# Optimization experiments

Measured on AMD Instinct MI355X. Metric: run time of the kernel, lower is better.

Reference implementation:

```python
import jax, jax.numpy as jnp
import numpy as np

DIM, E, K = 256, 8, 2
B, D, H, W = 1, 32, 32, 32
EPS = 1e-5


def setup_inputs() -> dict:
    key = jax.random.key(0)
    ks = jax.random.split(key, 16)
    nrm = lambda k, s, sc=0.02: jax.random.normal(k, s, jnp.float32) * sc
    def resblock_params(k):
        k1, k2, k3, k4 = jax.random.split(k, 4)
        return dict(
            c1w=nrm(k1, (DIM, DIM, 3, 3, 3)), c1b=jnp.zeros((DIM,), jnp.float32),
            g1=jax.random.uniform(k2, (DIM,), jnp.float32, 0.5, 1.5), be1=jnp.zeros((DIM,), jnp.float32),
            c2w=nrm(k3, (DIM, DIM, 3, 3, 3)), c2b=jnp.zeros((DIM,), jnp.float32),
            g2=jax.random.uniform(k4, (DIM,), jnp.float32, 0.5, 1.5), be2=jnp.zeros((DIM,), jnp.float32),
        )
    p1 = resblock_params(ks[5])
    p2 = resblock_params(ks[6])
    return {
        "x": jax.random.normal(ks[0], (B, DIM, D, H, W), jnp.float32),
        "wg": nrm(ks[1], (DIM, E)),
        "w1": nrm(ks[2], (E, DIM, DIM)), "b1": jnp.zeros((E, DIM), jnp.float32),
        "w2": nrm(ks[3], (E, DIM, DIM)), "b2": jnp.zeros((E, DIM), jnp.float32),
        "r1_c1w": p1["c1w"], "r1_c1b": p1["c1b"], "r1_g1": p1["g1"], "r1_be1": p1["be1"],
        "r1_c2w": p1["c2w"], "r1_c2b": p1["c2b"], "r1_g2": p1["g2"], "r1_be2": p1["be2"],
        "r2_c1w": p2["c1w"], "r2_c1b": p2["c1b"], "r2_g1": p2["g1"], "r2_be1": p2["be1"],
        "r2_c2w": p2["c2w"], "r2_c2b": p2["c2b"], "r2_g2": p2["g2"], "r2_be2": p2["be2"],
        "c8w": nrm(ks[4], (DIM, DIM, 1, 1, 1)), "c8b": jnp.zeros((DIM,), jnp.float32),
    }


def conv3d(x, w, b, pad):
    y = jax.lax.conv_general_dilated(
        x, w, window_strides=(1, 1, 1), padding=[(pad, pad)] * 3,
        dimension_numbers=("NCDHW", "OIDHW", "NCDHW"))
    return y + b[None, :, None, None, None]


def batchnorm(x, g, b):
    m = x.mean(axis=(0, 2, 3, 4), keepdims=True)
    v = x.var(axis=(0, 2, 3, 4), keepdims=True)
    return g[None, :, None, None, None] * (x - m) * jax.lax.rsqrt(v + EPS) + b[None, :, None, None, None]


def unet_res_block(x, c1w, c1b, g1, be1, c2w, c2b, g2, be2):
    out = jax.nn.leaky_relu(batchnorm(conv3d(x, c1w, c1b, 1), g1, be1), 0.01)
    out = batchnorm(conv3d(out, c2w, c2b, 1), g2, be2)
    return jax.nn.leaky_relu(out + x, 0.01)  # identity shortcut (in==out ch, stride 1)


def mom_block(x, wg, w1, b1, w2, b2):
    Bb, C, Dd, Hh, Ww = x.shape
    tokens = x.transpose(0, 2, 3, 4, 1).reshape(-1, C)  # [T, C]
    T = tokens.shape[0]
    probs = jax.nn.softmax(tokens @ wg, axis=-1)          # [T, E]
    vals, idx = jax.lax.top_k(probs, K)                   # [T, K]
    wts = vals / vals.sum(-1, keepdims=True)
    gates = jnp.zeros((T, E), probs.dtype).at[jnp.arange(T)[:, None], idx].set(wts)
    # dense expert MLPs (math-equivalent to gather/dispatch/combine)
    h = jax.nn.gelu(jnp.einsum("tc,ech->eth", tokens, w1) + b1[:, None, :])
    eo = jnp.einsum("eth,ehc->etc", h, w2) + b2[:, None, :]
    moe = jnp.einsum("te,etc->tc", gates, eo)             # [T, C]
    # switch-style load-balancing auxiliary loss
    density = (gates > 0).astype(probs.dtype).mean(0)     # fraction of tokens per expert
    density_proxy = probs.mean(0)
    aux = (density * density_proxy).sum() * E
    out = x + moe.reshape(Bb, Dd, Hh, Ww, C).transpose(0, 4, 1, 2, 3)
    return out, aux


def reference(x, wg, w1, b1, w2, b2,
              r1_c1w, r1_c1b, r1_g1, r1_be1, r1_c2w, r1_c2b, r1_g2, r1_be2,
              r2_c1w, r2_c1b, r2_g1, r2_be1, r2_c2w, r2_c2b, r2_g2, r2_be2,
              c8w, c8b):
    xm, aux = mom_block(x, wg, w1, b1, w2, b2)
    res = unet_res_block(xm, r1_c1w, r1_c1b, r1_g1, r1_be1, r1_c2w, r1_c2b, r1_g2, r1_be2)
    res = unet_res_block(res, r2_c1w, r2_c1b, r2_g1, r2_be1, r2_c2w, r2_c2b, r2_g2, r2_be2)
    out = xm + conv3d(res, c8w, c8b, 0)  # Dropout3d is identity at eval
    return out, aux
```

## Files before the change

### kernel.cpp

```cpp
#include <hip/hip_runtime.h>
#include <stdint.h>

typedef __attribute__((ext_vector_type(8))) short short8;
typedef __attribute__((ext_vector_type(4))) float f32x4;
typedef unsigned short u16;
typedef unsigned int u32;
typedef unsigned long long u64;

#define WS_TOK   0ull
#define WS_XT    16777216ull
#define WS_XMCT  50331648ull
#define WS_GATES 83886080ull
#define WS_H     84934656ull
#define WS_P1    135266304ull
#define WS_P2    155389952ull
#define WS_Y     175513600ull
#define WS_R2    209068032ull
#define WS_WRB   225845248ull
#define WS_W1P   240001024ull
#define WS_W2P   241049600ull
#define WS_C8P   242098176ull
#define WS_PART  242229248ull
#define WS_SF    243277824ull
#define WS_AUXP  243279872ull

#define WS_PERM  (WS_H + 0x00000ull)
#define WS_TBL   (WS_H + 0x60000ull)
#define WS_META  (WS_H + 0x70000ull)
#define WS_BCNT  (WS_H + 0x80000ull)
#define WS_BOFF  (WS_H + 0x90000ull)
#define WS_SEL   (WS_H + 0x100000ull)

__device__ __forceinline__ u16 f2bf(float f) {
  u32 x = __float_as_uint(f);
  u32 r = x + 0x7fffu + ((x >> 16) & 1u);
  return (u16)(r >> 16);
}

__global__ void trans_in_k(const float* __restrict__ x, float* __restrict__ xt,
                           u16* __restrict__ tok) {
  __shared__ float ld[64][65];
  int tt = blockIdx.x, cc = blockIdx.y, tid = threadIdx.x;
#pragma unroll
  for (int k = 0; k < 16; ++k) {
    int idx = tid + k * 256;
    int cl = idx >> 6, j = idx & 63;
    ld[cl][j] = x[(size_t)(cc * 64 + cl) * 32768 + tt * 64 + j];
  }
  __syncthreads();
#pragma unroll
  for (int k = 0; k < 16; ++k) {
    int idx = tid + k * 256;
    int tl = idx >> 6, cl = idx & 63;
    float v = ld[cl][tl];
    size_t o = (size_t)(tt * 64 + tl) * 256 + cc * 64 + cl;
    xt[o] = v;
    tok[o] = f2bf(v);
  }
}

__global__ void pack_rb_k(const float* __restrict__ w0, const float* __restrict__ w1,
                          const float* __restrict__ w2, const float* __restrict__ w3,
                          u16* __restrict__ out) {
  __shared__ float ld[6912];
  int conv = blockIdx.x >> 8, blk = blockIdx.x & 255, tid = threadIdx.x;
  const float* src = conv == 0 ? w0 : conv == 1 ? w1 : conv == 2 ? w2 : w3;
  size_t base = (size_t)blk * 256 * 27;
#pragma unroll
  for (int k = 0; k < 27; ++k) ld[tid + k * 256] = src[base + tid + k * 256];
  __syncthreads();
  u16* dst = out + (size_t)conv * 27 * 65536;
  int n = blk * 256 + tid;
#pragma unroll
  for (int tap = 0; tap < 27; ++tap)
    dst[(size_t)tap * 65536 + n] = f2bf(ld[tid * 27 + tap]);
}

__global__ void pack_tr_k(const float* __restrict__ w1, const float* __restrict__ w2,
                          u16* __restrict__ w1p, u16* __restrict__ w2p) {
  __shared__ float ld[64][65];
  int m = blockIdx.y, tile = blockIdx.x, tid = threadIdx.x;
  const float* src = (m < 8) ? (w1 + (size_t)m * 65536) : (w2 + (size_t)(m - 8) * 65536);
  u16* dst = (m < 8) ? (w1p + (size_t)m * 65536) : (w2p + (size_t)(m - 8) * 65536);
  int r0 = (tile >> 2) * 64, c0 = (tile & 3) * 64;
#pragma unroll
  for (int k = 0; k < 16; ++k) {
    int idx = tid + k * 256;
    int rr = idx >> 6, cc = idx & 63;
    ld[rr][cc] = src[(size_t)(r0 + rr) * 256 + c0 + cc];
  }
  __syncthreads();
#pragma unroll
  for (int k = 0; k < 16; ++k) {
    int idx = tid + k * 256;
    int cc = idx >> 6, rr = idx & 63;
    dst[(size_t)(c0 + cc) * 256 + r0 + rr] = f2bf(ld[rr][cc]);
  }
}

__global__ void cvt_k(const float* __restrict__ in, u16* __restrict__ out, int n) {
  int i = blockIdx.x * 256 + threadIdx.x;
  if (i < n) out[i] = f2bf(in[i]);
}

__global__ void halo_k(u16* __restrict__ P1, u16* __restrict__ P2) {
  int gid = blockIdx.x * 256 + threadIdx.x;
  int r = gid >> 5, o = (gid & 31) << 3;
  if (r >= 39304) return;
  int d = r / 1156, rem = r - d * 1156, h = rem / 34, w = rem - h * 34;
  if (d >= 1 && d <= 32 && h >= 1 && h <= 32 && w >= 1 && w <= 32) return;
  uint4 z = {0u, 0u, 0u, 0u};
  *(uint4*)(P1 + (size_t)r * 256 + o) = z;
  *(uint4*)(P2 + (size_t)r * 256 + o) = z;
}

__global__ void gate_k(const float* __restrict__ xt, const float* __restrict__ wg,
                       float* __restrict__ gw, u32* __restrict__ sel,
                       u32* __restrict__ blk_cnt, float* __restrict__ auxp) {
  __shared__ float wgs[2048];
  __shared__ float ax[4][16];
  __shared__ u32 bc[4][8];
  int tid = threadIdx.x;
#pragma unroll
  for (int k = 0; k < 8; ++k) wgs[tid + k * 256] = wg[tid + k * 256];
  __syncthreads();
  int t = blockIdx.x * 256 + tid;
  int lane = tid & 63, wv = tid >> 6;
  float l[8] = {0, 0, 0, 0, 0, 0, 0, 0};
  const float* xr = xt + (size_t)t * 256;
  for (int c = 0; c < 256; c += 4) {
    float4 xv = *(const float4*)(xr + c);
#pragma unroll
    for (int e = 0; e < 8; ++e)
      l[e] += xv.x * wgs[c * 8 + e] + xv.y * wgs[(c + 1) * 8 + e] +
              xv.z * wgs[(c + 2) * 8 + e] + xv.w * wgs[(c + 3) * 8 + e];
  }
  float mx = l[0];
#pragma unroll
  for (int e = 1; e < 8; ++e) mx = fmaxf(mx, l[e]);
  float p[8], sum = 0.f;
#pragma unroll
  for (int e = 0; e < 8; ++e) { p[e] = __expf(l[e] - mx); sum += p[e]; }
  float inv = 1.0f / sum;
#pragma unroll
  for (int e = 0; e < 8; ++e) p[e] *= inv;
  int i0 = 0; float v0 = p[0];
#pragma unroll
  for (int e = 1; e < 8; ++e) if (p[e] > v0) { v0 = p[e]; i0 = e; }
  int i1 = -1; float v1 = -1.0f;
#pragma unroll
  for (int e = 0; e < 8; ++e) if (e != i0 && p[e] > v1) { v1 = p[e]; i1 = e; }
  float wsum = v0 + v1;
  gw[t * 2] = v0 / wsum;
  gw[t * 2 + 1] = v1 / wsum;
  sel[t] = (u32)i0 | ((u32)i1 << 4);
  u64 mm[8];
#pragma unroll
  for (int e = 0; e < 8; ++e) mm[e] = __ballot(i0 == e || i1 == e);
  if (lane == 0) {
#pragma unroll
    for (int e = 0; e < 8; ++e) bc[wv][e] = (u32)__popcll(mm[e]);
  }
#pragma unroll
  for (int e = 0; e < 8; ++e) {
    float ps = p[e];
    float cn = (e == i0 || e == i1) ? 1.0f : 0.0f;
    for (int o = 32; o; o >>= 1) { ps += __shfl_down(ps, o); cn += __shfl_down(cn, o); }
    if (lane == 0) { ax[wv][e] = ps; ax[wv][8 + e] = cn; }
  }
  __syncthreads();
  if (tid < 16)
    auxp[blockIdx.x * 16 + tid] = ax[0][tid] + ax[1][tid] + ax[2][tid] + ax[3][tid];
  if (tid < 8)
    blk_cnt[blockIdx.x * 8 + tid] = bc[0][tid] + bc[1][tid] + bc[2][tid] + bc[3][tid];
}

__global__ void aux_k(const float* __restrict__ auxp, float* __restrict__ out) {
  __shared__ float s[16];
  int i = threadIdx.x;
  if (i < 16) {
    float a = 0;
    for (int b = 0; b < 128; ++b) a += auxp[b * 16 + i];
    s[i] = a;
  }
  __syncthreads();
  if (i == 0) {
    float r = 0;
    for (int e = 0; e < 8; ++e)
      r += (s[8 + e] * (1.0f / 32768.0f)) * (s[e] * (1.0f / 32768.0f));
    out[0] = r * 8.0f;
  }
}

__global__ void scan_k(const u32* __restrict__ blk_cnt, u32* __restrict__ blkoff,
                       u32* __restrict__ tbl, u32* __restrict__ meta,
                       u32* __restrict__ perm) {
  __shared__ u32 tot[8], base[8], nck[8], cbase[8];
  int tid = threadIdx.x;
  if (tid < 8) {
    u32 run = 0;
    for (int b = 0; b < 128; ++b) {
      blkoff[b * 8 + tid] = run;
      run += blk_cnt[b * 8 + tid];
    }
    tot[tid] = run;
  }
  __syncthreads();
  if (tid == 0) {
    u32 acc = 0, c = 0;
    for (int e = 0; e < 8; ++e) {
      base[e] = acc;
      u32 nc = (tot[e] + 127) >> 7;
      nck[e] = nc;
      cbase[e] = c;
      acc += nc << 7;
      c += nc;
    }
    meta[0] = c;
  }
  __syncthreads();
  for (int i = tid; i < 1024; i += 256) blkoff[i] += base[i & 7];
  if (tid < 8) {
    for (u32 k = 0; k < nck[tid]; ++k)
      tbl[cbase[tid] + k] = ((base[tid] + (k << 7)) << 4) | (u32)tid;
    for (u32 sl = base[tid] + tot[tid]; sl < base[tid] + (nck[tid] << 7); ++sl)
      perm[sl] = 0;
  }
}

__global__ void scatter_k(const u32* __restrict__ sel, const u32* __restrict__ blkoff,
                          u32* __restrict__ perm, u32* __restrict__ tpos) {
  __shared__ u32 wcnt[4][8];
  int tid = threadIdx.x, b = blockIdx.x;
  int lane = tid & 63, wv = tid >> 6;
  int t = b * 256 + tid;
  u32 s = sel[t];
  int i0 = s & 15, i1 = (s >> 4) & 15;
  u64 mm[8];
#pragma unroll
  for (int e = 0; e < 8; ++e) mm[e] = __ballot(i0 == e || i1 == e);
  if (lane == 0) {
#pragma unroll
    for (int e = 0; e < 8; ++e) wcnt[wv][e] = (u32)__popcll(mm[e]);
  }
  __syncthreads();
  u64 lt = (1ull << lane) - 1ull;
#pragma unroll
  for (int e = 0; e < 8; ++e) {
    bool is0 = (i0 == e), is1 = (i1 == e);
    if (is0 || is1) {
      u32 woff = 0;
#pragma unroll
      for (int w = 0; w < 4; ++w)
        if (w < wv) woff += wcnt[w][e];
      u32 pos = blkoff[b * 8 + e] + woff + (u32)__popcll(mm[e] & lt);
      perm[pos] = (u32)t;
      tpos[t * 2 + (is0 ? 0 : 1)] = pos;
    }
  }
}

__global__ __launch_bounds__(512, 2) void moe_gemm_k(
    const u16* __restrict__ tok, const u32* __restrict__ perm,
    const u32* __restrict__ tbl, const u32* __restrict__ meta,
    const u16* __restrict__ w1p, const u16* __restrict__ w2p,
    const float* __restrict__ b1, const float* __restrict__ b2,
    u16* __restrict__ eo) {
  __shared__ __attribute__((aligned(16))) unsigned char smem[163840];
  const int bid = blockIdx.x;
  if ((u32)bid >= meta[0]) return;
  const u32 ent = tbl[bid];
  const int e = (int)(ent & 15u);
  const int slot0 = (int)(ent >> 4);
  const int tid = threadIdx.x;
  const int lane = tid & 63;
  const int wv = tid >> 6;
  const int wr = (wv >> 2) * 64;
  const int wc = (wv & 3) * 64;
  const int fq = lane >> 4, fr = lane & 15;
  const u16* w1e = w1p + e * 65536;
  const u16* w2e = w2p + e * 65536;

#pragma unroll
  for (int it = 0; it < 8; ++it) {
    int s = tid + it * 512;
    int r = s >> 5, seg = s & 31;
    int cole = ((seg >> 3) << 6) + (((seg & 7) ^ (r & 7)) << 3);
    u32 rowtok = perm[slot0 + r];
    __builtin_amdgcn_global_load_lds(
        (const __attribute__((address_space(1))) u32*)(tok + (size_t)rowtok * 256 + cole),
        (__attribute__((address_space(3))) u32*)(smem + s * 16), 16, 0, 0);
  }

  f32x4 acc1[4][4];
#pragma unroll
  for (int mc = 0; mc < 4; ++mc)
#pragma unroll
    for (int nt = 0; nt < 4; ++nt) acc1[mc][nt] = (f32x4){0.f, 0.f, 0.f, 0.f};

#pragma unroll 1
  for (int kc = 0; kc < 4; ++kc) {
#pragma unroll
    for (int it = 0; it < 4; ++it) {
      int s = tid + it * 512;
      int r = s >> 3;
      int sub = (s & 7) ^ (r & 7);
      __builtin_amdgcn_global_load_lds(
          (const __attribute__((address_space(1))) u32*)(w1e + (size_t)r * 256 + kc * 64 + sub * 8),
          (__attribute__((address_space(3))) u32*)(smem + 65536 + s * 16), 16, 0, 0);
    }
    __syncthreads();
#pragma unroll
    for (int khf = 0; khf < 2; ++khf) {
      short8 af1[4], bt[4];
#pragma unroll
      for (int mc = 0; mc < 4; ++mc) {
        int row = wc + mc * 16 + fr;
        int p = (khf * 4 + fq) ^ (row & 7);
        af1[mc] = *(const short8*)(smem + 65536 + row * 128 + p * 16);
      }
#pragma unroll
      for (int nt = 0; nt < 4; ++nt) {
        int row = wr + nt * 16 + fr;
        int p = (khf * 4 + fq) ^ (row & 7);
        bt[nt] = *(const short8*)(smem + row * 512 + kc * 128 + p * 16);
      }
#pragma unroll
      for (int mc = 0; mc < 4; ++mc)
#pragma unroll
        for (int nt = 0; nt < 4; ++nt)
          acc1[mc][nt] = __builtin_amdgcn_mfma_f32_16x16x32_bf16(af1[mc], bt[nt], acc1[mc][nt], 0, 0, 0);
    }
    __syncthreads();
  }

#pragma unroll
  for (int mc = 0; mc < 4; ++mc) {
    int k0 = wc + mc * 16 + fq * 4;
    float4 bv = *(const float4*)(b1 + e * 256 + k0);
#pragma unroll
    for (int nt = 0; nt < 4; ++nt) {
      int t = wr + nt * 16 + fr;
      u64 pk = 0;
#pragma unroll
      for (int j = 0; j < 4; ++j) {
        float v = acc1[mc][nt][j] + ((const float*)&bv)[j];
        float u = 1.5957691216057308f * (v + 0.044715f * v * v * v);
        float g = v / (1.0f + __expf(-u));
        pk |= (u64)f2bf(g) << (16 * j);
      }
      *(u64*)(smem + 98304 + t * 512 + ((k0 * 2) ^ ((t & 7) << 4))) = pk;
    }
  }

  f32x4 acc2[4][4];
#pragma unroll
  for (int m = 0; m < 4; ++m)
#pragma unroll
    for (int n = 0; n < 4; ++n) acc2[m][n] = (f32x4){0.f, 0.f, 0.f, 0.f};

#pragma unroll 1
  for (int kc = 0; kc < 4; ++kc) {
#pragma unroll
    for (int it = 0; it < 4; ++it) {
      int s = tid + it * 512;
      int r = s >> 3;
      int sub = (s & 7) ^ (r & 7);
      __builtin_amdgcn_global_load_lds(
          (const __attribute__((address_space(1))) u32*)(w2e + (size_t)r * 256 + kc * 64 + sub * 8),
          (__attribute__((address_space(3))) u32*)(smem + 65536 + s * 16), 16, 0, 0);
    }
    __syncthreads();
#pragma unroll
    for (int khf = 0; khf < 2; ++khf) {
      short8 af[4], bb[4];
#pragma unroll
      for (int m = 0; m < 4; ++m) {
        int row = wr + m * 16 + fr;
        int col = (kc * 128 + (khf * 4 + fq) * 16) ^ ((row & 7) << 4);
        af[m] = *(const short8*)(smem + 98304 + row * 512 + col);
      }
#pragma unroll
      for (int n = 0; n < 4; ++n) {
        int row = wc + n * 16 + fr;
        int p = (khf * 4 + fq) ^ (row & 7);
        bb[n] = *(const short8*)(smem + 65536 + row * 128 + p * 16);
      }
#pragma unroll
      for (int m = 0; m < 4; ++m)
#pragma unroll
        for (int n = 0; n < 4; ++n)
          acc2[m][n] = __builtin_amdgcn_mfma_f32_16x16x32_bf16(af[m], bb[n], acc2[m][n], 0, 0, 0);
    }
    __syncthreads();
  }

  float bs2[4];
#pragma unroll
  for (int n = 0; n < 4; ++n) bs2[n] = b2[e * 256 + wc + n * 16 + fr];
#pragma unroll
  for (int m = 0; m < 4; ++m)
#pragma unroll
    for (int j = 0; j < 4; ++j) {
      int rowslot = slot0 + wr + m * 16 + fq * 4 + j;
      u16* er = eo + (size_t)rowslot * 256 + wc;
#pragma unroll
      for (int n = 0; n < 4; ++n) er[n * 16 + fr] = f2bf(acc2[m][n][j] + bs2[n]);
    }
}

__global__ void combine_k(float* __restrict__ xt, const u16* __restrict__ eo,
                          const float* __restrict__ gw, const u32* __restrict__ tpos,
                          float* __restrict__ xmct, u16* __restrict__ pad) {
  __shared__ float ld[64][65];
  __shared__ u32 pp[64][2];
  __shared__ float gg[64][2];
  int tt = blockIdx.x, cc = blockIdx.y, tid = threadIdx.x;
  if (tid < 128) {
    int tl = tid >> 1, s = tid & 1;
    int t = tt * 64 + tl;
    pp[tl][s] = tpos[t * 2 + s];
    gg[tl][s] = gw[t * 2 + s];
  }
  __syncthreads();
#pragma unroll
  for (int k = 0; k < 16; ++k) {
    int idx = tid + k * 256;
    int tl = idx >> 6, cl = idx & 63;
    int c = cc * 64 + cl;
    size_t o = (size_t)(tt * 64 + tl) * 256 + c;
    float e0 = __uint_as_float((u32)eo[(size_t)pp[tl][0] * 256 + c] << 16);
    float e1 = __uint_as_float((u32)eo[(size_t)pp[tl][1] * 256 + c] << 16);
    float v = xt[o] + gg[tl][0] * e0 + gg[tl][1] * e1;
    xt[o] = v;
    ld[tl][cl] = v;
    int t = tt * 64 + tl;
    int d = t >> 10, h = (t >> 5) & 31, w = t & 31;
    int prow = (d + 1) * 1156 + (h + 1) * 34 + (w + 1);
    pad[(size_t)prow * 256 + c] = f2bf(v);
  }
  __syncthreads();
#pragma unroll
  for (int k = 0; k < 16; ++k) {
    int idx = tid + k * 256;
    int cl = idx >> 6, tl = idx & 63;
    xmct[(size_t)(cc * 64 + cl) * 32768 + tt * 64 + tl] = ld[tl][cl];
  }
}

template <int MODE>
__global__ __launch_bounds__(256, 2) void gemm_k(
    const u16* __restrict__ A, const u16* __restrict__ Bw,
    const float* __restrict__ bias, float* __restrict__ outF,
    const float* __restrict__ xmct, float* __restrict__ part) {
  __shared__ __attribute__((aligned(16))) unsigned char smem[65536];
  const int tid = threadIdx.x;
  const int bx = blockIdx.x;
  const int ttile = (MODE == 0) ? ((bx & 7) * 32 + (bx >> 3)) : bx;
  const int ctile = blockIdx.y;
  const int lane = tid & 63;
  const int wv = tid >> 6;
  const int wr = (wv >> 1) << 6;
  const int wc = (wv & 1) << 6;
  const int fq = lane >> 4;
  const int fr = lane & 15;

  int aoff[4], boff[4];
#pragma unroll
  for (int it = 0; it < 4; ++it) {
    int s = tid + it * 256;
    int r = s >> 3;
    int lsg = (s & 7) ^ (r & 7);
    if (MODE == 0) {
      int dd = ttile >> 3;
      int h0 = (ttile & 7) << 2;
      int base = dd * 1156 + (h0 + (r >> 5)) * 34 + (r & 31);
      aoff[it] = base * 256 + lsg * 8;
    } else {
      aoff[it] = (ttile * 128 + r) * 256 + lsg * 8;
    }
    boff[it] = (ctile * 128 + r) * 256 + lsg * 8;
  }

  f32x4 acc[4][4];
#pragma unroll
  for (int m = 0; m < 4; ++m)
#pragma unroll
    for (int n = 0; n < 4; ++n) acc[m][n] = (f32x4){0.f, 0.f, 0.f, 0.f};

  const int nStep = (MODE == 0) ? 108 : 4;

  auto stage = [&](int s, int buf) {
    int tap = (MODE == 0) ? (s >> 2) : 0;
    int kc = s & 3;
    int atap = 0, btap = 0;
    if (MODE == 0) {
      atap = ((tap / 9) * 1156 + ((tap / 3) % 3) * 34 + (tap % 3)) * 256;
      btap = tap * 65536;
    }
    const u16* Ak = A + atap + kc * 64;
    const u16* Bk = Bw + btap + kc * 64;
    unsigned char* sb = smem + buf * 32768;
#pragma unroll
    for (int it = 0; it < 4; ++it) {
      __builtin_amdgcn_global_load_lds(
          (const __attribute__((address_space(1))) u32*)(Ak + aoff[it]),
          (__attribute__((address_space(3))) u32*)(sb + (tid + it * 256) * 16),
          16, 0, 0);
      __builtin_amdgcn_global_load_lds(
          (const __attribute__((address_space(1))) u32*)(Bk + boff[it]),
          (__attribute__((address_space(3))) u32*)(sb + 16384 + (tid + it * 256) * 16),
          16, 0, 0);
    }
  };

  auto compute = [&](int buf) {
    unsigned char* sb = smem + buf * 32768;
#pragma unroll
    for (int khf = 0; khf < 2; ++khf) {
      short8 af[4], bb[4];
#pragma unroll
      for (int m = 0; m < 4; ++m) {
        int row = wr + m * 16 + fr;
        int p = (khf * 4 + fq) ^ (row & 7);
        af[m] = *(const short8*)(sb + row * 128 + p * 16);
      }
#pragma unroll
      for (int n = 0; n < 4; ++n) {
        int row = wc + n * 16 + fr;
        int p = (khf * 4 + fq) ^ (row & 7);
        bb[n] = *(const short8*)(sb + 16384 + row * 128 + p * 16);
      }
#pragma unroll
      for (int m = 0; m < 4; ++m)
#pragma unroll
        for (int n = 0; n < 4; ++n)
          acc[m][n] = __builtin_amdgcn_mfma_f32_16x16x32_bf16(af[m], bb[n], acc[m][n], 0, 0, 0);
    }
  };

  stage(0, 0);
  asm volatile("s_waitcnt vmcnt(0)" ::: "memory");
  __builtin_amdgcn_s_barrier();
  int cur = 0;
#pragma unroll 1
  for (int s = 0; s < nStep; ++s) {
    if (s + 1 < nStep) stage(s + 1, cur ^ 1);
    compute(cur);
    asm volatile("s_waitcnt vmcnt(0)" ::: "memory");
    __builtin_amdgcn_s_barrier();
    cur ^= 1;
  }

  float bs[4];
#pragma unroll
  for (int n = 0; n < 4; ++n) bs[n] = bias[ctile * 128 + wc + n * 16 + fr];

  if (MODE == 3) {
#pragma unroll
    for (int m = 0; m < 4; ++m) {
      int trow = ttile * 128 + wr + m * 16 + fq * 4;
#pragma unroll
      for (int n = 0; n < 4; ++n) {
        int oc = ctile * 128 + wc + n * 16 + fr;
        size_t o = (size_t)oc * 32768 + trow;
        float4 xv = *(const float4*)(xmct + o);
        float4 w;
        w.x = acc[m][n][0] + bs[n] + xv.x;
        w.y = acc[m][n][1] + bs[n] + xv.y;
        w.z = acc[m][n][2] + bs[n] + xv.z;
        w.w = acc[m][n][3] + bs[n] + xv.w;
        *(float4*)(outF + o) = w;
      }
    }
  } else {
    float sn[4] = {0, 0, 0, 0}, qn[4] = {0, 0, 0, 0};
#pragma unroll
    for (int m = 0; m < 4; ++m) {
#pragma unroll
      for (int j = 0; j < 4; ++j) {
        int t = ttile * 128 + wr + m * 16 + fq * 4 + j;
        float* yr = outF + (size_t)t * 256 + ctile * 128 + wc;
#pragma unroll
        for (int n = 0; n < 4; ++n) {
          float v = acc[m][n][j] + bs[n];
          yr[n * 16 + fr] = v;
          sn[n] += v;
          qn[n] += v * v;
        }
      }
    }
#pragma unroll
    for (int n = 0; n < 4; ++n) {
      float s = sn[n], q = qn[n];
      s += __shfl_xor(s, 16); s += __shfl_xor(s, 32);
      q += __shfl_xor(q, 16); q += __shfl_xor(q, 32);
      if (lane < 16) {
        int pi = (ttile * 2 + (wv >> 1)) * 256 + ctile * 128 + wc + n * 16 + fr;
        part[pi] = s;
        part[131072 + pi] = q;
      }
    }
  }
}

__global__ void stats2_k(const float* __restrict__ part, const float* __restrict__ g,
                         const float* __restrict__ be, float* __restrict__ sf) {
  __shared__ float sred[4][256], qred[4][256];
  int tid = threadIdx.x;
  int c = tid & 255, qd = tid >> 8;
  float s = 0, q = 0;
  for (int b = qd * 128; b < qd * 128 + 128; ++b) {
    s += part[b * 256 + c];
    q += part[131072 + b * 256 + c];
  }
  sred[qd][c] = s;
  qred[qd][c] = q;
  __syncthreads();
  if (qd == 0) {
    s = sred[0][c] + sred[1][c] + sred[2][c] + sred[3][c];
    q = qred[0][c] + qred[1][c] + qred[2][c] + qred[3][c];
    float mean = s * (1.0f / 32768.0f);
    float var = q * (1.0f / 32768.0f) - mean * mean;
    float a = g[c] * rsqrtf(var + 1e-5f);
    sf[c] = a;
    sf[256 + c] = be[c] - mean * a;
  }
}

template <int V>
__global__ void bn_k(const float* __restrict__ y, const float* __restrict__ sf,
                     const float* __restrict__ skip, u16* __restrict__ pad,
                     float* __restrict__ f32o, u16* __restrict__ bfo) {
  int gid = blockIdx.x * 256 + threadIdx.x;
  int t = gid >> 5, c0 = (gid & 31) << 3;
  size_t base = (size_t)t * 256 + c0;
  float v[8];
  const float4* yp = (const float4*)(y + base);
  float4 y0 = yp[0], y1 = yp[1];
  const float4* ap = (const float4*)(sf + c0);
  float4 a0 = ap[0], a1 = ap[1];
  const float4* shp = (const float4*)(sf + 256 + c0);
  float4 s0 = shp[0], s1 = shp[1];
  v[0] = a0.x * y0.x + s0.x; v[1] = a0.y * y0.y + s0.y;
  v[2] = a0.z * y0.z + s0.z; v[3] = a0.w * y0.w + s0.w;
  v[4] = a1.x * y1.x + s1.x; v[5] = a1.y * y1.y + s1.y;
  v[6] = a1.z * y1.z + s1.z; v[7] = a1.w * y1.w + s1.w;
  if (V >= 1) {
    const float4* kp = (const float4*)(skip + base);
    float4 k0 = kp[0], k1 = kp[1];
    v[0] += k0.x; v[1] += k0.y; v[2] += k0.z; v[3] += k0.w;
    v[4] += k1.x; v[5] += k1.y; v[6] += k1.z; v[7] += k1.w;
  }
#pragma unroll
  for (int i = 0; i < 8; ++i) v[i] = v[i] > 0.0f ? v[i] : 0.01f * v[i];
  if (V <= 1) {
    int d = t >> 10, h = (t >> 5) & 31, w = t & 31;
    int prow = (d + 1) * 1156 + (h + 1) * 34 + (w + 1);
    uint4 pk;
    pk.x = (u32)f2bf(v[0]) | ((u32)f2bf(v[1]) << 16);
    pk.y = (u32)f2bf(v[2]) | ((u32)f2bf(v[3]) << 16);
    pk.z = (u32)f2bf(v[4]) | ((u32)f2bf(v[5]) << 16);
    pk.w = (u32)f2bf(v[6]) | ((u32)f2bf(v[7]) << 16);
    *(uint4*)(pad + (size_t)prow * 256 + c0) = pk;
  }
  if (V == 1) {
    float4 o0 = {v[0], v[1], v[2], v[3]}, o1 = {v[4], v[5], v[6], v[7]};
    float4* fp = (float4*)(f32o + base);
    fp[0] = o0; fp[1] = o1;
  }
  if (V == 2) {
    uint4 pk;
    pk.x = (u32)f2bf(v[0]) | ((u32)f2bf(v[1]) << 16);
    pk.y = (u32)f2bf(v[2]) | ((u32)f2bf(v[3]) << 16);
    pk.z = (u32)f2bf(v[4]) | ((u32)f2bf(v[5]) << 16);
    pk.w = (u32)f2bf(v[6]) | ((u32)f2bf(v[7]) << 16);
    *(uint4*)(bfo + base) = pk;
  }
}

extern "C" void kernel_launch(void* const* d_in, const int* in_sizes, int n_in,
                              void* d_out, int out_size, void* d_ws, size_t ws_size,
                              hipStream_t stream) {
  (void)in_sizes; (void)n_in; (void)out_size; (void)ws_size;
  const float* x  = (const float*)d_in[0];
  const float* wg = (const float*)d_in[1];
  const float* w1 = (const float*)d_in[2];
  const float* b1 = (const float*)d_in[3];
  const float* w2 = (const float*)d_in[4];
  const float* b2 = (const float*)d_in[5];

  char* ws = (char*)d_ws;
  u16* tok    = (u16*)(ws + WS_TOK);
  float* xt   = (float*)(ws + WS_XT);
  float* xmct = (float*)(ws + WS_XMCT);
  float* gw   = (float*)(ws + WS_GATES);
  u32* tpos   = (u32*)(ws + WS_GATES + 0x80000ull);
  u32* perm   = (u32*)(ws + WS_PERM);
  u32* tbl    = (u32*)(ws + WS_TBL);
  u32* meta   = (u32*)(ws + WS_META);
  u32* bcnt   = (u32*)(ws + WS_BCNT);
  u32* boff   = (u32*)(ws + WS_BOFF);
  u32* selb   = (u32*)(ws + WS_SEL);
  u16* P1     = (u16*)(ws + WS_P1);
  u16* P2     = (u16*)(ws + WS_P2);
  float* ybuf = (float*)(ws + WS_Y);
  u16* eo     = (u16*)(ws + WS_Y);
  u16* r2b    = (u16*)(ws + WS_R2);
  u16* wrb    = (u16*)(ws + WS_WRB);
  u16* w1p    = (u16*)(ws + WS_W1P);
  u16* w2p    = (u16*)(ws + WS_W2P);
  u16* c8p    = (u16*)(ws + WS_C8P);
  float* part = (float*)(ws + WS_PART);
  float* sf   = (float*)(ws + WS_SF);
  float* auxp = (float*)(ws + WS_AUXP);
  float* outp = (float*)d_out;

  halo_k<<<4913, 256, 0, stream>>>(P1, P2);
  trans_in_k<<<dim3(512, 4), 256, 0, stream>>>(x, xt, tok);
  pack_rb_k<<<1024, 256, 0, stream>>>((const float*)d_in[6], (const float*)d_in[10],
                                      (const float*)d_in[14], (const float*)d_in[18], wrb);
  pack_tr_k<<<dim3(16, 16), 256, 0, stream>>>(w1, w2, w1p, w2p);
  cvt_k<<<256, 256, 0, stream>>>((const float*)d_in[22], c8p, 65536);

  gate_k<<<128, 256, 0, stream>>>(xt, wg, gw, selb, bcnt, auxp);
  scan_k<<<1, 256, 0, stream>>>(bcnt, boff, tbl, meta, perm);
  scatter_k<<<128, 256, 0, stream>>>(selb, boff, perm, tpos);
  moe_gemm_k<<<520, 512, 0, stream>>>(tok, perm, tbl, meta, w1p, w2p, b1, b2, eo);
  combine_k<<<dim3(512, 4), 256, 0, stream>>>(xt, eo, gw, tpos, xmct, P1);

  gemm_k<0><<<dim3(256, 2), 256, 0, stream>>>(P1, wrb + 0 * 1769472, (const float*)d_in[7],
                                              ybuf, nullptr, part);
  stats2_k<<<1, 1024, 0, stream>>>(part, (const float*)d_in[8], (const float*)d_in[9], sf);
  bn_k<0><<<4096, 256, 0, stream>>>(ybuf, sf, nullptr, P2, nullptr, nullptr);
  gemm_k<0><<<dim3(256, 2), 256, 0, stream>>>(P2, wrb + 1 * 1769472, (const float*)d_in[11],
                                              ybuf, nullptr, part);
  stats2_k<<<1, 1024, 0, stream>>>(part, (const float*)d_in[12], (const float*)d_in[13], sf);
  bn_k<1><<<4096, 256, 0, stream>>>(ybuf, sf, xt, P1, xt, nullptr);

  gemm_k<0><<<dim3(256, 2), 256, 0, stream>>>(P1, wrb + 2 * 1769472, (const float*)d_in[15],
                                              ybuf, nullptr, part);
  stats2_k<<<1, 1024, 0, stream>>>(part, (const float*)d_in[16], (const float*)d_in[17], sf);
  bn_k<0><<<4096, 256, 0, stream>>>(ybuf, sf, nullptr, P2, nullptr, nullptr);
  gemm_k<0><<<dim3(256, 2), 256, 0, stream>>>(P2, wrb + 3 * 1769472, (const float*)d_in[19],
                                              ybuf, nullptr, part);
  stats2_k<<<1, 1024, 0, stream>>>(part, (const float*)d_in[20], (const float*)d_in[21], sf);
  bn_k<2><<<4096, 256, 0, stream>>>(ybuf, sf, xt, nullptr, nullptr, r2b);

  gemm_k<3><<<dim3(256, 2), 256, 0, stream>>>(r2b, c8p, (const float*)d_in[23], outp,
                                              xmct, nullptr);
  aux_k<<<1, 64, 0, stream>>>(auxp, outp + 8388608);
}
```

Measured before the change: 713.8 us.

## Widen conv GEMM to full 256 output channels with triple-buffered pipeline and bf16 output

Replaces the 3x3x3 conv GEMM with a dedicated 512-thread kernel that computes all 256 output channels per token tile. This halves redundant loads of the padded activation tile, and each stage's global-to-LDS loads are split across the two k-halves behind a three-deep buffer ring, with MFMA priority raised. The conv output is now stored as bf16 instead of fp32, which halves intermediate traffic read back by the batchnorm kernel. The trade-off is lower BN input precision, one block per CU with heavy LDS use, and fewer blocks (256) to fill the device.

```diff
diff --git a/kernel.cpp b/kernel.cpp
--- a/kernel.cpp
+++ b/kernel.cpp
@@ -36,6 +36,7 @@
   u32 r = x + 0x7fffu + ((x >> 16) & 1u);
   return (u16)(r >> 16);
 }
+__device__ __forceinline__ float bf2f(u32 u) { return __uint_as_float(u << 16); }
 
 __global__ void trans_in_k(const float* __restrict__ x, float* __restrict__ xt,
                            u16* __restrict__ tok) {
@@ -429,8 +430,8 @@
     int tl = idx >> 6, cl = idx & 63;
     int c = cc * 64 + cl;
     size_t o = (size_t)(tt * 64 + tl) * 256 + c;
-    float e0 = __uint_as_float((u32)eo[(size_t)pp[tl][0] * 256 + c] << 16);
-    float e1 = __uint_as_float((u32)eo[(size_t)pp[tl][1] * 256 + c] << 16);
+    float e0 = bf2f(eo[(size_t)pp[tl][0] * 256 + c]);
+    float e1 = bf2f(eo[(size_t)pp[tl][1] * 256 + c]);
     float v = xt[o] + gg[tl][0] * e0 + gg[tl][1] * e1;
     xt[o] = v;
     ld[tl][cl] = v;
@@ -448,15 +449,159 @@
   }
 }
 
-template <int MODE>
-__global__ __launch_bounds__(256, 2) void gemm_k(
+__global__ __launch_bounds__(512, 1) void conv_k(
+    const u16* __restrict__ P, const u16* __restrict__ W,
+    const float* __restrict__ bias, u16* __restrict__ y,
+    float* __restrict__ part) {
+  __shared__ __attribute__((aligned(16))) unsigned char smem[147456];
+  const int tid = threadIdx.x;
+  const int bx = blockIdx.x;
+  const int ttile = (bx & 7) * 32 + (bx >> 3);
+  const int lane = tid & 63;
+  const int wv = tid >> 6;
+  const int wr = (wv >> 2) << 6;
+  const int wc = (wv & 3) << 6;
+  const int fq = lane >> 4, fr = lane & 15;
+  const int dd = ttile >> 3, h0 = (ttile & 7) << 2;
+
+  int goffA[2];
+#pragma unroll
+  for (int it = 0; it < 2; ++it) {
+    int s = tid + it * 512;
+    int r = s >> 3, c = s & 7;
+    int base = dd * 1156 + (h0 + (r >> 5)) * 34 + (r & 31);
+    goffA[it] = base * 256 + ((c ^ (r & 7)) << 3);
+  }
+  int goffB[4];
+#pragma unroll
+  for (int it = 0; it < 4; ++it) {
+    int s = tid + it * 512;
+    int r = s >> 3, c = s & 7;
+    goffB[it] = r * 256 + ((c ^ (r & 7)) << 3);
+  }
+
+  f32x4 acc[4][4];
+#pragma unroll
+  for (int m = 0; m < 4; ++m)
+#pragma unroll
+    for (int n = 0; n < 4; ++n) acc[m][n] = (f32x4){0.f, 0.f, 0.f, 0.f};
+
+#define CONV_STAGE(s2, half)                                                        \
+  {                                                                                 \
+    int tap_ = (s2) >> 2, kc_ = (s2) & 3;                                           \
+    int aofs_ = ((tap_ / 9) * 1156 + ((tap_ / 3) % 3) * 34 + (tap_ % 3)) * 256 +    \
+                kc_ * 64;                                                           \
+    int bofs_ = tap_ * 65536 + kc_ * 64;                                            \
+    unsigned char* sb_ = smem + ((s2) % 3) * 49152;                                 \
+    if ((half) == 0) {                                                              \
+      __builtin_amdgcn_global_load_lds(                                             \
+          (const __attribute__((address_space(1))) u32*)(P + aofs_ + goffA[0]),     \
+          (__attribute__((address_space(3))) u32*)(sb_ + tid * 16), 16, 0, 0);      \
+      __builtin_amdgcn_global_load_lds(                                             \
+          (const __attribute__((address_space(1))) u32*)(P + aofs_ + goffA[1]),     \
+          (__attribute__((address_space(3))) u32*)(sb_ + (tid + 512) * 16), 16, 0, 0); \
+      __builtin_amdgcn_global_load_lds(                                             \
+          (const __attribute__((address_space(1))) u32*)(W + bofs_ + goffB[0]),     \
+          (__attribute__((address_space(3))) u32*)(sb_ + 16384 + tid * 16), 16, 0, 0); \
+    } else {                                                                        \
+      __builtin_amdgcn_global_load_lds(                                             \
+          (const __attribute__((address_space(1))) u32*)(W + bofs_ + goffB[1]),     \
+          (__attribute__((address_space(3))) u32*)(sb_ + 16384 + (tid + 512) * 16), \
+          16, 0, 0);                                                                \
+      __builtin_amdgcn_global_load_lds(                                             \
+          (const __attribute__((address_space(1))) u32*)(W + bofs_ + goffB[2]),     \
+          (__attribute__((address_space(3))) u32*)(sb_ + 16384 + (tid + 1024) * 16),\
+          16, 0, 0);                                                                \
+      __builtin_amdgcn_global_load_lds(                                             \
+          (const __attribute__((address_space(1))) u32*)(W + bofs_ + goffB[3]),     \
+          (__attribute__((address_space(3))) u32*)(sb_ + 16384 + (tid + 1536) * 16),\
+          16, 0, 0);                                                                \
+    }                                                                               \
+  }
+
+  CONV_STAGE(0, 0); CONV_STAGE(0, 1);
+  CONV_STAGE(1, 0); CONV_STAGE(1, 1);
+  asm volatile("s_waitcnt vmcnt(6)" ::: "memory");
+  __builtin_amdgcn_s_barrier();
+
+#pragma unroll 1
+  for (int s = 0; s < 108; ++s) {
+    const unsigned char* sb = smem + (s % 3) * 49152;
+    const bool doStage = (s < 106);
+#pragma unroll
+    for (int khf = 0; khf < 2; ++khf) {
+      short8 af[4], bb[4];
+#pragma unroll
+      for (int m = 0; m < 4; ++m) {
+        int row = wr + m * 16 + fr;
+        int p = (khf * 4 + fq) ^ (row & 7);
+        af[m] = *(const short8*)(sb + row * 128 + p * 16);
+      }
+#pragma unroll
+      for (int n = 0; n < 4; ++n) {
+        int row = wc + n * 16 + fr;
+        int p = (khf * 4 + fq) ^ (row & 7);
+        bb[n] = *(const short8*)(sb + 16384 + row * 128 + p * 16);
+      }
+      if (doStage) CONV_STAGE(s + 2, khf);
+      __builtin_amdgcn_s_barrier();
+      __builtin_amdgcn_s_setprio(1);
+#pragma unroll
+      for (int m = 0; m < 4; ++m)
+#pragma unroll
+        for (int n = 0; n < 4; ++n)
+          acc[m][n] = __builtin_amdgcn_mfma_f32_16x16x32_bf16(af[m], bb[n], acc[m][n], 0, 0, 0);
+      __builtin_amdgcn_s_setprio(0);
+      if (khf == 0) __builtin_amdgcn_s_barrier();
+    }
+    if (doStage)
+      asm volatile("s_waitcnt vmcnt(6)" ::: "memory");
+    else
+      asm volatile("s_waitcnt vmcnt(0)" ::: "memory");
+    __builtin_amdgcn_s_barrier();
+  }
+#undef CONV_STAGE
+
+  float bs[4];
+#pragma unroll
+  for (int n = 0; n < 4; ++n) bs[n] = bias[wc + n * 16 + fr];
+
+  float sn[4] = {0, 0, 0, 0}, qn[4] = {0, 0, 0, 0};
+#pragma unroll
+  for (int m = 0; m < 4; ++m) {
+#pragma unroll
+    for (int j = 0; j < 4; ++j) {
+      int t = ttile * 128 + wr + m * 16 + fq * 4 + j;
+      u16* yr = y + (size_t)t * 256 + wc;
+#pragma unroll
+      for (int n = 0; n < 4; ++n) {
+        float v = acc[m][n][j] + bs[n];
+        yr[n * 16 + fr] = f2bf(v);
+        sn[n] += v;
+        qn[n] += v * v;
+      }
+    }
+  }
+#pragma unroll
+  for (int n = 0; n < 4; ++n) {
+    float s = sn[n], q = qn[n];
+    s += __shfl_xor(s, 16); s += __shfl_xor(s, 32);
+    q += __shfl_xor(q, 16); q += __shfl_xor(q, 32);
+    if (lane < 16) {
+      int pi = (ttile * 2 + (wv >> 2)) * 256 + wc + n * 16 + fr;
+      part[pi] = s;
+      part[131072 + pi] = q;
+    }
+  }
+}
+
+__global__ __launch_bounds__(256, 2) void final_k(
     const u16* __restrict__ A, const u16* __restrict__ Bw,
     const float* __restrict__ bias, float* __restrict__ outF,
-    const float* __restrict__ xmct, float* __restrict__ part) {
+    const float* __restrict__ xmct) {
   __shared__ __attribute__((aligned(16))) unsigned char smem[65536];
   const int tid = threadIdx.x;
-  const int bx = blockIdx.x;
-  const int ttile = (MODE == 0) ? ((bx & 7) * 32 + (bx >> 3)) : bx;
+  const int ttile = blockIdx.x;
   const int ctile = blockIdx.y;
   const int lane = tid & 63;
   const int wv = tid >> 6;
@@ -471,14 +616,7 @@
     int s = tid + it * 256;
     int r = s >> 3;
     int lsg = (s & 7) ^ (r & 7);
-    if (MODE == 0) {
-      int dd = ttile >> 3;
-      int h0 = (ttile & 7) << 2;
-      int base = dd * 1156 + (h0 + (r >> 5)) * 34 + (r & 31);
-      aoff[it] = base * 256 + lsg * 8;
-    } else {
-      aoff[it] = (ttile * 128 + r) * 256 + lsg * 8;
-    }
+    aoff[it] = (ttile * 128 + r) * 256 + lsg * 8;
     boff[it] = (ctile * 128 + r) * 256 + lsg * 8;
   }
 
@@ -488,18 +626,9 @@
 #pragma unroll
     for (int n = 0; n < 4; ++n) acc[m][n] = (f32x4){0.f, 0.f, 0.f, 0.f};
 
-  const int nStep = (MODE == 0) ? 108 : 4;
-
-  auto stage = [&](int s, int buf) {
-    int tap = (MODE == 0) ? (s >> 2) : 0;
-    int kc = s & 3;
-    int atap = 0, btap = 0;
-    if (MODE == 0) {
-      atap = ((tap / 9) * 1156 + ((tap / 3) % 3) * 34 + (tap % 3)) * 256;
-      btap = tap * 65536;
-    }
-    const u16* Ak = A + atap + kc * 64;
-    const u16* Bk = Bw + btap + kc * 64;
+  auto stage = [&](int kc, int buf) {
+    const u16* Ak = A + kc * 64;
+    const u16* Bk = Bw + kc * 64;
     unsigned char* sb = smem + buf * 32768;
 #pragma unroll
     for (int it = 0; it < 4; ++it) {
@@ -513,7 +642,6 @@
           16, 0, 0);
     }
   };
-
   auto compute = [&](int buf) {
     unsigned char* sb = smem + buf * 32768;
 #pragma unroll
@@ -544,8 +672,8 @@
   __builtin_amdgcn_s_barrier();
   int cur = 0;
 #pragma unroll 1
-  for (int s = 0; s < nStep; ++s) {
-    if (s + 1 < nStep) stage(s + 1, cur ^ 1);
+  for (int s = 0; s < 4; ++s) {
+    if (s + 1 < 4) stage(s + 1, cur ^ 1);
     compute(cur);
     asm volatile("s_waitcnt vmcnt(0)" ::: "memory");
     __builtin_amdgcn_s_barrier();
@@ -556,50 +684,20 @@
 #pragma unroll
   for (int n = 0; n < 4; ++n) bs[n] = bias[ctile * 128 + wc + n * 16 + fr];
 
-  if (MODE == 3) {
-#pragma unroll
-    for (int m = 0; m < 4; ++m) {
-      int trow = ttile * 128 + wr + m * 16 + fq * 4;
-#pragma unroll
-      for (int n = 0; n < 4; ++n) {
-        int oc = ctile * 128 + wc + n * 16 + fr;
-        size_t o = (size_t)oc * 32768 + trow;
-        float4 xv = *(const float4*)(xmct + o);
-        float4 w;
-        w.x = acc[m][n][0] + bs[n] + xv.x;
-        w.y = acc[m][n][1] + bs[n] + xv.y;
-        w.z = acc[m][n][2] + bs[n] + xv.z;
-        w.w = acc[m][n][3] + bs[n] + xv.w;
-        *(float4*)(outF + o) = w;
-      }
-    }
-  } else {
-    float sn[4] = {0, 0, 0, 0}, qn[4] = {0, 0, 0, 0};
-#pragma unroll
-    for (int m = 0; m < 4; ++m) {
-#pragma unroll
-      for (int j = 0; j < 4; ++j) {
-        int t = ttile * 128 + wr + m * 16 + fq * 4 + j;
-        float* yr = outF + (size_t)t * 256 + ctile * 128 + wc;
-#pragma unroll
-        for (int n = 0; n < 4; ++n) {
-          float v = acc[m][n][j] + bs[n];
-          yr[n * 16 + fr] = v;
-          sn[n] += v;
-          qn[n] += v * v;
-        }
-      }
-    }
+#pragma unroll
+  for (int m = 0; m < 4; ++m) {
+    int trow = ttile * 128 + wr + m * 16 + fq * 4;
 #pragma unroll
     for (int n = 0; n < 4; ++n) {
-      float s = sn[n], q = qn[n];
-      s += __shfl_xor(s, 16); s += __shfl_xor(s, 32);
-      q += __shfl_xor(q, 16); q += __shfl_xor(q, 32);
-      if (lane < 16) {
-        int pi = (ttile * 2 + (wv >> 1)) * 256 + ctile * 128 + wc + n * 16 + fr;
-        part[pi] = s;
-        part[131072 + pi] = q;
-      }
+      int oc = ctile * 128 + wc + n * 16 + fr;
+      size_t o = (size_t)oc * 32768 + trow;
+      float4 xv = *(const float4*)(xmct + o);
+      float4 w;
+      w.x = acc[m][n][0] + bs[n] + xv.x;
+      w.y = acc[m][n][1] + bs[n] + xv.y;
+      w.z = acc[m][n][2] + bs[n] + xv.z;
+      w.w = acc[m][n][3] + bs[n] + xv.w;
+      *(float4*)(outF + o) = w;
     }
   }
 }
@@ -629,23 +727,26 @@
 }
 
 template <int V>
-__global__ void bn_k(const float* __restrict__ y, const float* __restrict__ sf,
+__global__ void bn_k(const u16* __restrict__ y, const float* __restrict__ sf,
                      const float* __restrict__ skip, u16* __restrict__ pad,
                      float* __restrict__ f32o, u16* __restrict__ bfo) {
   int gid = blockIdx.x * 256 + threadIdx.x;
   int t = gid >> 5, c0 = (gid & 31) << 3;
   size_t base = (size_t)t * 256 + c0;
   float v[8];
-  const float4* yp = (const float4*)(y + base);
-  float4 y0 = yp[0], y1 = yp[1];
+  uint4 yv = *(const uint4*)(y + base);
+  v[0] = bf2f(yv.x & 0xffffu); v[1] = bf2f(yv.x >> 16);
+  v[2] = bf2f(yv.y & 0xffffu); v[3] = bf2f(yv.y >> 16);
+  v[4] = bf2f(yv.z & 0xffffu); v[5] = bf2f(yv.z >> 16);
+  v[6] = bf2f(yv.w & 0xffffu); v[7] = bf2f(yv.w >> 16);
   const float4* ap = (const float4*)(sf + c0);
   float4 a0 = ap[0], a1 = ap[1];
   const float4* shp = (const float4*)(sf + 256 + c0);
   float4 s0 = shp[0], s1 = shp[1];
-  v[0] = a0.x * y0.x + s0.x; v[1] = a0.y * y0.y + s0.y;
-  v[2] = a0.z * y0.z + s0.z; v[3] = a0.w * y0.w + s0.w;
-  v[4] = a1.x * y1.x + s1.x; v[5] = a1.y * y1.y + s1.y;
-  v[6] = a1.z * y1.z + s1.z; v[7] = a1.w * y1.w + s1.w;
+  v[0] = a0.x * v[0] + s0.x; v[1] = a0.y * v[1] + s0.y;
+  v[2] = a0.z * v[2] + s0.z; v[3] = a0.w * v[3] + s0.w;
+  v[4] = a1.x * v[4] + s1.x; v[5] = a1.y * v[5] + s1.y;
+  v[6] = a1.z * v[6] + s1.z; v[7] = a1.w * v[7] + s1.w;
   if (V >= 1) {
     const float4* kp = (const float4*)(skip + base);
     float4 k0 = kp[0], k1 = kp[1];
@@ -704,7 +805,7 @@
   u32* selb   = (u32*)(ws + WS_SEL);
   u16* P1     = (u16*)(ws + WS_P1);
   u16* P2     = (u16*)(ws + WS_P2);
-  float* ybuf = (float*)(ws + WS_Y);
+  u16* ybuf   = (u16*)(ws + WS_Y);
   u16* eo     = (u16*)(ws + WS_Y);
   u16* r2b    = (u16*)(ws + WS_R2);
   u16* wrb    = (u16*)(ws + WS_WRB);
@@ -729,25 +830,20 @@
   moe_gemm_k<<<520, 512, 0, stream>>>(tok, perm, tbl, meta, w1p, w2p, b1, b2, eo);
   combine_k<<<dim3(512, 4), 256, 0, stream>>>(xt, eo, gw, tpos, xmct, P1);
 
-  gemm_k<0><<<dim3(256, 2), 256, 0, stream>>>(P1, wrb + 0 * 1769472, (const float*)d_in[7],
-                                              ybuf, nullptr, part);
+  conv_k<<<256, 512, 0, stream>>>(P1, wrb + 0 * 1769472, (const float*)d_in[7], ybuf, part);
   stats2_k<<<1, 1024, 0, stream>>>(part, (const float*)d_in[8], (const float*)d_in[9], sf);
   bn_k<0><<<4096, 256, 0, stream>>>(ybuf, sf, nullptr, P2, nullptr, nullptr);
-  gemm_k<0><<<dim3(256, 2), 256, 0, stream>>>(P2, wrb + 1 * 1769472, (const float*)d_in[11],
-                                              ybuf, nullptr, part);
+  conv_k<<<256, 512, 0, stream>>>(P2, wrb + 1 * 1769472, (const float*)d_in[11], ybuf, part);
   stats2_k<<<1, 1024, 0, stream>>>(part, (const float*)d_in[12], (const float*)d_in[13], sf);
   bn_k<1><<<4096, 256, 0, stream>>>(ybuf, sf, xt, P1, xt, nullptr);
 
-  gemm_k<0><<<dim3(256, 2), 256, 0, stream>>>(P1, wrb + 2 * 1769472, (const float*)d_in[15],
-                                              ybuf, nullptr, part);
+  conv_k<<<256, 512, 0, stream>>>(P1, wrb + 2 * 1769472, (const float*)d_in[15], ybuf, part);
   stats2_k<<<1, 1024, 0, stream>>>(part, (const float*)d_in[16], (const float*)d_in[17], sf);
   bn_k<0><<<4096, 256, 0, stream>>>(ybuf, sf, nullptr, P2, nullptr, nullptr);
-  gemm_k<0><<<dim3(256, 2), 256, 0, stream>>>(P2, wrb + 3 * 1769472, (const float*)d_in[19],
-                                              ybuf, nullptr, part);
+  conv_k<<<256, 512, 0, stream>>>(P2, wrb + 3 * 1769472, (const float*)d_in[19], ybuf, part);
   stats2_k<<<1, 1024, 0, stream>>>(part, (const float*)d_in[20], (const float*)d_in[21], sf);
   bn_k<2><<<4096, 256, 0, stream>>>(ybuf, sf, xt, nullptr, nullptr, r2b);
 
-  gemm_k<3><<<dim3(256, 2), 256, 0, stream>>>(r2b, c8p, (const float*)d_in[23], outp,
-                                              xmct, nullptr);
+  final_k<<<dim3(256, 2), 256, 0, stream>>>(r2b, c8p, (const float*)d_in[23], outp, xmct);
   aux_k<<<1, 64, 0, stream>>>(auxp, outp + 8388608);
 }
```

New measurement: 737.9 us. 1.03x slower.
